# Kernel optimization log

Hardware: AMD Instinct MI355X
Metric: run time of the kernel (lower is better)

## Reference

```python
import jax, jax.numpy as jnp
import numpy as np

N_NODES = 100000
N_EDGES = 3200000
D = 256
REPEAT = 2
FACTOR = 0.5


def setup_inputs() -> dict:
    key = jax.random.key(0)
    k1, k2, k3, k4, k5, k6 = jax.random.split(key, 6)
    x = jax.random.normal(k1, (N_NODES, D), dtype=jnp.float32)
    vals = jax.random.uniform(k2, (N_EDGES,), dtype=jnp.float32)
    # Xavier-ish scale for linear weights
    W0 = jax.random.normal(k3, (D, D), dtype=jnp.float32) / np.sqrt(D)
    W1 = jax.random.normal(k4, (D, D), dtype=jnp.float32) / np.sqrt(D)
    rows = jax.random.randint(k5, (N_EDGES,), 0, N_NODES, dtype=jnp.int32)
    cols = jax.random.randint(k6, (N_EDGES,), 0, N_NODES, dtype=jnp.int32)
    return {"x": x, "vals": vals, "W0": W0, "W1": W1, "rows": rows, "cols": cols}


def reference(x, vals, W0, W1, rows, cols):
    # support is sparse [N, N] in COO: support[rows[e], cols[e]] = vals[e]
    def spmm(h):
        # gather source-node features, scale by edge weight, scatter-add to dst
        return jax.ops.segment_sum(vals[:, None] * h[cols], rows,
                                   num_segments=N_NODES)

    h = x
    for W, act in ((W0, jax.nn.relu), (W1, lambda v: v)):
        # _propagate: repeated SpMM with scalar factor
        for _ in range(REPEAT):
            h = spmm(h) * FACTOR
        # linear (no bias) + activation
        h = act(h @ W)
    return h
```

## Files before the change

kernel.cpp:

```cpp
#include <hip/hip_runtime.h>
#include <hip/hip_bf16.h>
#include <hip/hip_fp16.h>

#define N_D 256
#define NBLK 832
#define CPB 52
#define NCH 16
#define RPG_MAX 12512
#define EPB 4096
#define PR 512

typedef __attribute__((ext_vector_type(8))) short bf16x8;
typedef __attribute__((ext_vector_type(4))) float f32x4;

__device__ __forceinline__ unsigned short f2bf(float f) {
  union { float f; unsigned u; } c; c.f = f;
  unsigned u = c.u;
  return (unsigned short)((u + 0x7fffu + ((u >> 16) & 1u)) >> 16);
}
__device__ __forceinline__ float asf(unsigned u) {
  union { unsigned u; float f; } c; c.u = u;
  return c.f;
}
__device__ __forceinline__ int grp_of(int r, unsigned gmagic) {
  int g = (int)(((unsigned long long)(unsigned)r * gmagic) >> 37);
  return min(g, 7);
}
__device__ __forceinline__ unsigned packcv(int c, float vl) {
  const unsigned short hb = __half_as_ushort(__float2half_rn(vl * 0.5f));
  return ((unsigned)c << 15) | ((unsigned)hb >> 1);
}

template <bool AF32>
__device__ __forceinline__ void gemm_core(
    const void* __restrict__ H, const unsigned short* __restrict__ WT,
    unsigned short* __restrict__ C, int M, int bid) {
  const int wave = threadIdx.x >> 6;
  const int lane = threadIdx.x & 63;
  const int m = lane & 15;
  const int p = lane >> 4;
  const int row0 = bid * 128 + wave * 32;

  f32x4 acc0[16], acc1[16];
#pragma unroll
  for (int i = 0; i < 16; ++i) {
    acc0[i] = (f32x4){0.f, 0.f, 0.f, 0.f};
    acc1[i] = (f32x4){0.f, 0.f, 0.f, 0.f};
  }

  const int r0 = row0 + m;
  const int r1 = row0 + 16 + m;
  const bool ok0 = r0 < M, ok1 = r1 < M;

  for (int k0 = 0; k0 < N_D; k0 += 32) {
    bf16x8 a0 = {0,0,0,0,0,0,0,0}, a1 = {0,0,0,0,0,0,0,0};
    if (AF32) {
      if (ok0) {
        const float* ap = (const float*)H + (size_t)r0 * N_D + k0 + p * 8;
        const float4 f0 = *reinterpret_cast<const float4*>(ap);
        const float4 f1 = *reinterpret_cast<const float4*>(ap + 4);
        a0[0]=f2bf(f0.x); a0[1]=f2bf(f0.y); a0[2]=f2bf(f0.z); a0[3]=f2bf(f0.w);
        a0[4]=f2bf(f1.x); a0[5]=f2bf(f1.y); a0[6]=f2bf(f1.z); a0[7]=f2bf(f1.w);
      }
      if (ok1) {
        const float* ap = (const float*)H + (size_t)r1 * N_D + k0 + p * 8;
        const float4 f0 = *reinterpret_cast<const float4*>(ap);
        const float4 f1 = *reinterpret_cast<const float4*>(ap + 4);
        a1[0]=f2bf(f0.x); a1[1]=f2bf(f0.y); a1[2]=f2bf(f0.z); a1[3]=f2bf(f0.w);
        a1[4]=f2bf(f1.x); a1[5]=f2bf(f1.y); a1[6]=f2bf(f1.z); a1[7]=f2bf(f1.w);
      }
    } else {
      if (ok0) a0 = *reinterpret_cast<const bf16x8*>(
          (const unsigned short*)H + (size_t)r0 * N_D + k0 + p * 8);
      if (ok1) a1 = *reinterpret_cast<const bf16x8*>(
          (const unsigned short*)H + (size_t)r1 * N_D + k0 + p * 8);
    }
#pragma unroll
    for (int nt = 0; nt < 16; ++nt) {
      const bf16x8 b = *reinterpret_cast<const bf16x8*>(
          WT + (size_t)(nt * 16 + m) * N_D + k0 + p * 8);
      acc0[nt] = __builtin_amdgcn_mfma_f32_16x16x32_bf16(a0, b, acc0[nt], 0, 0, 0);
      acc1[nt] = __builtin_amdgcn_mfma_f32_16x16x32_bf16(a1, b, acc1[nt], 0, 0, 0);
    }
  }

#pragma unroll
  for (int nt = 0; nt < 16; ++nt) {
    const int col = nt * 16 + m;
#pragma unroll
    for (int rr = 0; rr < 4; ++rr) {
      const int ra = row0 + p * 4 + rr;
      const int rb = ra + 16;
      if (ra < M) C[(size_t)ra * N_D + col] = f2bf(acc0[nt][rr]);
      if (rb < M) C[(size_t)rb * N_D + col] = f2bf(acc1[nt][rr]);
    }
  }
}

__global__ __launch_bounds__(256) void gemm3_f32(
    const float* __restrict__ H, const unsigned short* __restrict__ WT,
    unsigned short* __restrict__ C, int M) {
  gemm_core<true>(H, WT, C, M, blockIdx.x);
}
__global__ __launch_bounds__(256) void gemm3_bf16(
    const unsigned short* __restrict__ H, const unsigned short* __restrict__ WT,
    unsigned short* __restrict__ C, int M) {
  gemm_core<false>(H, WT, C, M, blockIdx.x);
}

__global__ __launch_bounds__(256) void p0_kernel(
    const int* __restrict__ rows, int* __restrict__ cntT,
    int n_edges, unsigned gmagic,
    const float* __restrict__ W0, const float* __restrict__ W1,
    unsigned short* __restrict__ WT0, unsigned short* __restrict__ WT1) {
  if (blockIdx.x >= NBLK) {
    const int b = blockIdx.x - NBLK;
    const int w = b >> 8;
    const int k = b & 255;
    const int n = threadIdx.x;
    const float* W = w ? W1 : W0;
    unsigned short* WT = w ? WT1 : WT0;
    WT[(size_t)n * N_D + k] = f2bf(W[(size_t)k * N_D + n]);
    return;
  }
  __shared__ int l8[8];
  if (threadIdx.x < 8) l8[threadIdx.x] = 0;
  __syncthreads();
  const int e0 = blockIdx.x * EPB;
  const int e1 = min(n_edges, e0 + EPB);
  for (int e = e0 + threadIdx.x * 4; e < e1; e += 1024) {
    if (e + 3 < e1) {
      const int4 v = *reinterpret_cast<const int4*>(rows + e);
      atomicAdd(&l8[grp_of(v.x, gmagic)], 1);
      atomicAdd(&l8[grp_of(v.y, gmagic)], 1);
      atomicAdd(&l8[grp_of(v.z, gmagic)], 1);
      atomicAdd(&l8[grp_of(v.w, gmagic)], 1);
    } else {
      for (int k = 0; k < 4 && e + k < e1; ++k)
        atomicAdd(&l8[grp_of(rows[e + k], gmagic)], 1);
    }
  }
  __syncthreads();
  if (threadIdx.x < 8) cntT[threadIdx.x * NBLK + blockIdx.x] = l8[threadIdx.x];
}

__global__ __launch_bounds__(256) void scan_one(
    const int* __restrict__ in, int* __restrict__ out, int n) {
  __shared__ int swsum[4];
  __shared__ int carry_sh;
  const int tid = threadIdx.x;
  const int lane = tid & 63;
  const int wid = tid >> 6;
  if (tid == 0) carry_sh = 0;
  __syncthreads();
  for (int base = 0; base < n; base += 1024) {
    const int i0 = base + tid * 4;
    int4 v = make_int4(0, 0, 0, 0);
    if (i0 + 3 < n) v = *reinterpret_cast<const int4*>(in + i0);
    else {
      if (i0     < n) v.x = in[i0];
      if (i0 + 1 < n) v.y = in[i0 + 1];
      if (i0 + 2 < n) v.z = in[i0 + 2];
    }
    const int s1 = v.x, s2 = s1 + v.y, s3 = s2 + v.z, s4 = s3 + v.w;
    int ws = s4;
#pragma unroll
    for (int off = 1; off < 64; off <<= 1) {
      int o = __shfl_up(ws, off, 64);
      if (lane >= off) ws += o;
    }
    if (lane == 63) swsum[wid] = ws;
    __syncthreads();
    if (wid == 0) {
      int t = (lane < 4) ? swsum[lane] : 0;
#pragma unroll
      for (int off = 1; off < 4; off <<= 1) {
        int o = __shfl_up(t, off, 64);
        if (lane >= off) t += o;
      }
      if (lane < 4) swsum[lane] = t;
    }
    __syncthreads();
    const int carry = carry_sh;
    const int tbase = carry + (wid ? swsum[wid - 1] : 0) + ws - s4;
    if (i0     < n) out[i0]     = tbase;
    if (i0 + 1 < n) out[i0 + 1] = tbase + s1;
    if (i0 + 2 < n) out[i0 + 2] = tbase + s2;
    if (i0 + 3 < n) out[i0 + 3] = tbase + s3;
    __syncthreads();
    if (tid == 0) carry_sh = carry + swsum[3];
    __syncthreads();
  }
  if (tid == 0) out[n] = carry_sh;
}

__global__ __launch_bounds__(256) void partition_kernel(
    const int* __restrict__ rows, const int* __restrict__ cols,
    const float* __restrict__ vals, const int* __restrict__ pofsT,
    int2* __restrict__ part, int n_edges, unsigned gmagic) {
  __shared__ int lofs[8];
  __shared__ int lcnt[8];
  __shared__ int2 lbuf[8][PR];
  const int tid = threadIdx.x;
  const int bid = blockIdx.x;
  if (tid < 8) lofs[tid] = pofsT[tid * NBLK + bid];
  const int e0 = bid * EPB;
  const int e1 = min(n_edges, e0 + EPB);
  for (int base = e0; base < e1; base += PR) {
    if (tid < 8) lcnt[tid] = 0;
    __syncthreads();
    const int e = base + tid * 2;
    if (e < e1) {
      int2 rr, cc; float2 vv;
      const bool two = (e + 1 < e1);
      if (two) {
        rr = *reinterpret_cast<const int2*>(rows + e);
        cc = *reinterpret_cast<const int2*>(cols + e);
        vv = *reinterpret_cast<const float2*>(vals + e);
      } else {
        rr.x = rows[e]; cc.x = cols[e]; vv.x = vals[e];
      }
      {
        const int g = grp_of(rr.x, gmagic);
        const int slot = atomicAdd(&lcnt[g], 1);
        lbuf[g][slot] = make_int2(rr.x, (int)packcv(cc.x, vv.x));
      }
      if (two) {
        const int g = grp_of(rr.y, gmagic);
        const int slot = atomicAdd(&lcnt[g], 1);
        lbuf[g][slot] = make_int2(rr.y, (int)packcv(cc.y, vv.y));
      }
    }
    __syncthreads();
    for (int g = 0; g < 8; ++g) {
      const int c = lcnt[g];
      const int o = lofs[g];
      for (int i = tid; i < c; i += 256) part[o + i] = lbuf[g][i];
    }
    __syncthreads();
    if (tid < 8) lofs[tid] += lcnt[tid];
  }
}

__global__ __launch_bounds__(256) void hist_kernel(
    const int2* __restrict__ part, const int* __restrict__ pofsT,
    int* __restrict__ cntc, int M, int rpg) {
  const int g = blockIdx.x & 7;
  const int b = blockIdx.x >> 3;
  const int r0 = g * rpg;
  const int nr = min(rpg, M - r0);
  __shared__ int lh[RPG_MAX];
  for (int r = threadIdx.x; r < nr; r += 256) lh[r] = 0;
  __syncthreads();
  const int s0 = pofsT[g * NBLK + b * CPB];
  const int s1 = pofsT[g * NBLK + (b + 1) * CPB];
  for (int i = s0 + threadIdx.x; i < s1; i += 256) {
    atomicAdd(&lh[part[i].x - r0], 1);
  }
  __syncthreads();
  int* dst = cntc + (size_t)(g * NCH + b) * rpg;
  for (int r = threadIdx.x; r < nr; r += 256) dst[r] = lh[r];
}

__global__ __launch_bounds__(256) void sumcnt2_kernel(
    int* __restrict__ cntc, int* __restrict__ cnts,
    int* __restrict__ bsum, int M, int rpg) {
  __shared__ int wred[4];
  const int i = blockIdx.x * 256 + threadIdx.x;
  int s = 0;
  if (i < M) {
    const int g = i / rpg;
    const int rr = i - g * rpg;
    int* base = cntc + (size_t)g * NCH * rpg + rr;
#pragma unroll
    for (int b = 0; b < NCH; ++b) {
      const int c = base[(size_t)b * rpg];
      base[(size_t)b * rpg] = s;
      s += c;
    }
    cnts[i] = s;
  }
  int t = s;
#pragma unroll
  for (int off = 32; off; off >>= 1) t += __shfl_down(t, off, 64);
  if ((threadIdx.x & 63) == 0) wred[threadIdx.x >> 6] = t;
  __syncthreads();
  if (threadIdx.x == 0) bsum[blockIdx.x] = wred[0] + wred[1] + wred[2] + wred[3];
}

__global__ __launch_bounds__(256) void apply_kernel(
    const int* __restrict__ cnts, const int* __restrict__ bofs,
    int* __restrict__ row_ptr, int M) {
  __shared__ int wsum[4];
  const int tid = threadIdx.x;
  const int lane = tid & 63;
  const int wid = tid >> 6;
  const int i = blockIdx.x * 256 + tid;
  const int v = (i < M) ? cnts[i] : 0;
  int s = v;
#pragma unroll
  for (int off = 1; off < 64; off <<= 1) {
    int o = __shfl_up(s, off, 64);
    if (lane >= off) s += o;
  }
  if (lane == 63) wsum[wid] = s;
  __syncthreads();
  int add = 0;
  for (int k = 0; k < wid; ++k) add += wsum[k];
  const int excl = bofs[blockIdx.x] + add + s - v;
  if (i < M) row_ptr[i] = excl;
  if (i == M) row_ptr[M] = bofs[gridDim.x];
}

__global__ __launch_bounds__(256) void scatter3_kernel(
    const int2* __restrict__ part, const int* __restrict__ pofsT,
    const int* __restrict__ row_ptr, const int* __restrict__ cntc,
    unsigned* __restrict__ colpack, int M, int rpg) {
  const int g = blockIdx.x & 7;
  const int b = blockIdx.x >> 3;
  const int r0 = g * rpg;
  const int nr = min(rpg, M - r0);
  __shared__ int lc[RPG_MAX];
  const int* pfx = cntc + (size_t)(g * NCH + b) * rpg;
  for (int r = threadIdx.x; r < nr; r += 256)
    lc[r] = row_ptr[r0 + r] + pfx[r];
  __syncthreads();
  const int s0 = pofsT[g * NBLK + b * CPB];
  const int s1 = pofsT[g * NBLK + (b + 1) * CPB];
  for (int i = s0 + threadIdx.x; i < s1; i += 256) {
    const int2 rv = part[i];
    const int pos = atomicAdd(&lc[rv.x - r0], 1);
    colpack[pos] = (unsigned)rv.y;
  }
}

template <bool RELU, bool F32OUT>
__global__ __launch_bounds__(256) void spmm_slice(
    const unsigned short* __restrict__ hin, const int* __restrict__ row_ptr,
    const unsigned* __restrict__ colpack, void* __restrict__ hout,
    int n_nodes) {
  const int slice = blockIdx.x & 3;
  const int lane = threadIdx.x & 63;
  const int half = lane >> 5;
  const int sub  = lane & 31;
  const int wgid = ((blockIdx.x >> 2) * 256 + threadIdx.x) >> 6;
  const int node = wgid * 2 + half;
  const bool ok = node < n_nodes;
  int start = 0, end = 0;
  if (ok) { start = row_ptr[node]; end = row_ptr[node + 1]; }

  const unsigned* __restrict__ hinw = reinterpret_cast<const unsigned*>(hin);
  const int fofs = slice * 32 + sub;
  const int sbase = half << 5;

  float acc0 = 0.f, acc1 = 0.f;

  for (int base = start; base < end; base += 32) {
    const int cnt = min(32, end - base);
    unsigned u = 0;
    if (base + sub < end) u = __builtin_nontemporal_load(&colpack[base + sub]);
    for (int t = 0; t < cnt; t += 8) {
      unsigned hv[8];
      float v[8];
#pragma unroll
      for (int j = 0; j < 8; ++j) {
        const unsigned ue = (unsigned)__shfl((int)u, sbase + t + j, 64);
        const int c = (int)(ue >> 15);
        v[j] = __half2float(__ushort_as_half((unsigned short)(ue << 1)));
        hv[j] = hinw[(size_t)c * 128 + fofs];
      }
#pragma unroll
      for (int j = 0; j < 8; ++j) {
        acc0 += v[j] * asf(hv[j] << 16);
        acc1 += v[j] * asf(hv[j] & 0xffff0000u);
      }
    }
  }
  if (ok) {
    if (RELU) { acc0 = fmaxf(acc0, 0.f); acc1 = fmaxf(acc1, 0.f); }
    if (F32OUT) {
      reinterpret_cast<float2*>(hout)[(size_t)node * 128 + fofs] =
          make_float2(acc0, acc1);
    } else {
      reinterpret_cast<unsigned*>(hout)[(size_t)node * 128 + fofs] =
          (unsigned)f2bf(acc0) | ((unsigned)f2bf(acc1) << 16);
    }
  }
}

extern "C" void kernel_launch(void* const* d_in, const int* in_sizes, int n_in,
                              void* d_out, int out_size, void* d_ws, size_t ws_size,
                              hipStream_t stream) {
  const float* x    = (const float*)d_in[0];
  const float* vals = (const float*)d_in[1];
  const float* W0   = (const float*)d_in[2];
  const float* W1   = (const float*)d_in[3];
  const int*   rows = (const int*)d_in[4];
  const int*   cols = (const int*)d_in[5];

  const int n_edges = in_sizes[1];
  const int M = in_sizes[0] / N_D;
  const size_t n_feat = (size_t)M * N_D;

  char* ws = (char*)d_ws;
  unsigned short* hA      = (unsigned short*)(ws);
  unsigned*       colpack = (unsigned*)(ws + 51200000);
  int*            row_ptr = (int*)(ws + 64000000);
  int*            cnts    = (int*)(ws + 64400128);
  int*            bsum    = (int*)(ws + 64800256);
  int*            bofs    = (int*)(ws + 64802816);
  int*            cntT    = (int*)(ws + 64805376);
  int*            pofsT   = (int*)(ws + 64832000);
  unsigned short* wt0     = (unsigned short*)(ws + 64858880);
  unsigned short* wt1     = (unsigned short*)(ws + 64989952);
  unsigned short* hB   = (unsigned short*)d_out;
  unsigned short* hC   = (unsigned short*)d_out + n_feat;
  int2*           part = (int2*)((char*)d_out + 51200000);
  int*            cntc = (int*)((char*)d_out + 76800000);

  const int Mb = (M + 255) / 256;
  const int sblocks = 4 * ((M + 7) / 8);
  const int gblocks = (M + 127) / 128;
  const int rpg = (M + 7) / 8;
  const unsigned gmagic = (unsigned)(((1ULL << 37) + rpg - 1) / (unsigned long long)rpg);

  p0_kernel<<<NBLK + 512, 256, 0, stream>>>(rows, cntT, n_edges, gmagic,
                                            W0, W1, wt0, wt1);
  scan_one<<<1, 256, 0, stream>>>(cntT, pofsT, 8 * NBLK);
  gemm3_f32<<<gblocks, 256, 0, stream>>>(x, wt0, hB, M);
  partition_kernel<<<NBLK, 256, 0, stream>>>(rows, cols, vals, pofsT, part,
                                             n_edges, gmagic);
  hist_kernel<<<8 * NCH, 256, 0, stream>>>(part, pofsT, cntc, M, rpg);
  sumcnt2_kernel<<<Mb, 256, 0, stream>>>(cntc, cnts, bsum, M, rpg);
  scan_one<<<1, 256, 0, stream>>>(bsum, bofs, Mb);
  apply_kernel<<<Mb, 256, 0, stream>>>(cnts, bofs, row_ptr, M);
  scatter3_kernel<<<8 * NCH, 256, 0, stream>>>(part, pofsT, row_ptr, cntc,
                                               colpack, M, rpg);

  spmm_slice<false, false><<<sblocks, 256, 0, stream>>>(hB, row_ptr, colpack, hA, M);
  spmm_slice<true,  false><<<sblocks, 256, 0, stream>>>(hA, row_ptr, colpack, hB, M);

  gemm3_bf16<<<gblocks, 256, 0, stream>>>(hB, wt1, hC, M);
  spmm_slice<false, false><<<sblocks, 256, 0, stream>>>(hC, row_ptr, colpack, hA, M);
  spmm_slice<false, true ><<<sblocks, 256, 0, stream>>>(hA, row_ptr, colpack, d_out, M);
}
```

Before: 1.059 ms.

## Replace three-kernel row_ptr scan with per-group scan using partition offsets

Replaces the sumcnt/scan_one/apply kernel chain with a single 8-block groupscan kernel. Each block computes the degrees for its row group, scans them locally starting from the group's partition base offset in pofsT, and writes both row_ptr and absolute per-chunk offsets into cntc, so scatter no longer needs to read row_ptr. The GEMM A-operand loads also switch to nontemporal loads. This removes two launches and one grid-wide dependency, but the scan now runs on only 8 blocks with a serial per-thread chunk.

```diff
diff --git a/kernel.cpp b/kernel.cpp
--- a/kernel.cpp
+++ b/kernel.cpp
@@ -56,24 +56,24 @@
     bf16x8 a0 = {0,0,0,0,0,0,0,0}, a1 = {0,0,0,0,0,0,0,0};
     if (AF32) {
       if (ok0) {
-        const float* ap = (const float*)H + (size_t)r0 * N_D + k0 + p * 8;
-        const float4 f0 = *reinterpret_cast<const float4*>(ap);
-        const float4 f1 = *reinterpret_cast<const float4*>(ap + 4);
+        const f32x4* ap = (const f32x4*)((const float*)H + (size_t)r0 * N_D + k0 + p * 8);
+        const f32x4 f0 = __builtin_nontemporal_load(ap);
+        const f32x4 f1 = __builtin_nontemporal_load(ap + 1);
         a0[0]=f2bf(f0.x); a0[1]=f2bf(f0.y); a0[2]=f2bf(f0.z); a0[3]=f2bf(f0.w);
         a0[4]=f2bf(f1.x); a0[5]=f2bf(f1.y); a0[6]=f2bf(f1.z); a0[7]=f2bf(f1.w);
       }
       if (ok1) {
-        const float* ap = (const float*)H + (size_t)r1 * N_D + k0 + p * 8;
-        const float4 f0 = *reinterpret_cast<const float4*>(ap);
-        const float4 f1 = *reinterpret_cast<const float4*>(ap + 4);
+        const f32x4* ap = (const f32x4*)((const float*)H + (size_t)r1 * N_D + k0 + p * 8);
+        const f32x4 f0 = __builtin_nontemporal_load(ap);
+        const f32x4 f1 = __builtin_nontemporal_load(ap + 1);
         a1[0]=f2bf(f0.x); a1[1]=f2bf(f0.y); a1[2]=f2bf(f0.z); a1[3]=f2bf(f0.w);
         a1[4]=f2bf(f1.x); a1[5]=f2bf(f1.y); a1[6]=f2bf(f1.z); a1[7]=f2bf(f1.w);
       }
     } else {
-      if (ok0) a0 = *reinterpret_cast<const bf16x8*>(
-          (const unsigned short*)H + (size_t)r0 * N_D + k0 + p * 8);
-      if (ok1) a1 = *reinterpret_cast<const bf16x8*>(
-          (const unsigned short*)H + (size_t)r1 * N_D + k0 + p * 8);
+      if (ok0) a0 = __builtin_nontemporal_load(reinterpret_cast<const bf16x8*>(
+          (const unsigned short*)H + (size_t)r0 * N_D + k0 + p * 8));
+      if (ok1) a1 = __builtin_nontemporal_load(reinterpret_cast<const bf16x8*>(
+          (const unsigned short*)H + (size_t)r1 * N_D + k0 + p * 8));
     }
 #pragma unroll
     for (int nt = 0; nt < 16; ++nt) {
@@ -262,68 +262,76 @@
   for (int r = threadIdx.x; r < nr; r += 256) dst[r] = lh[r];
 }
 
-__global__ __launch_bounds__(256) void sumcnt2_kernel(
-    int* __restrict__ cntc, int* __restrict__ cnts,
-    int* __restrict__ bsum, int M, int rpg) {
-  __shared__ int wred[4];
-  const int i = blockIdx.x * 256 + threadIdx.x;
+__global__ __launch_bounds__(256) void groupscan_kernel(
+    int* __restrict__ cntc, const int* __restrict__ pofsT,
+    int* __restrict__ row_ptr, int M, int rpg) {
+  const int g = blockIdx.x;
+  const int r0 = g * rpg;
+  const int nr = min(rpg, M - r0);
+  __shared__ int deg[RPG_MAX];
+  __shared__ int tsum[256];
+  __shared__ int wq[4];
+  const int tid = threadIdx.x;
+  int* base = cntc + (size_t)g * NCH * rpg;
+  for (int r = tid; r < nr; r += 256) {
+    int s = 0;
+#pragma unroll
+    for (int b = 0; b < NCH; ++b) s += base[(size_t)b * rpg + r];
+    deg[r] = s;
+  }
+  __syncthreads();
+  const int CH = (nr + 255) / 256;
+  const int a0 = min(nr, tid * CH);
+  const int a1 = min(nr, a0 + CH);
   int s = 0;
-  if (i < M) {
-    const int g = i / rpg;
-    const int rr = i - g * rpg;
-    int* base = cntc + (size_t)g * NCH * rpg + rr;
+  for (int r = a0; r < a1; ++r) s += deg[r];
+  {
+    const int lane = tid & 63, wid = tid >> 6;
+    int sc = s;
+#pragma unroll
+    for (int off = 1; off < 64; off <<= 1) {
+      int o = __shfl_up(sc, off, 64);
+      if (lane >= off) sc += o;
+    }
+    if (lane == 63) wq[wid] = sc;
+    __syncthreads();
+    int add = 0;
+    for (int k = 0; k < wid; ++k) add += wq[k];
+    tsum[tid] = add + sc - s;
+  }
+  __syncthreads();
+  const int gbase = pofsT[g * NBLK];
+  int run = gbase + tsum[tid];
+  for (int r = a0; r < a1; ++r) {
+    const int d = deg[r];
+    deg[r] = run;
+    run += d;
+  }
+  __syncthreads();
+  for (int r = tid; r < nr; r += 256) {
+    int acc = deg[r];
+    row_ptr[r0 + r] = acc;
 #pragma unroll
     for (int b = 0; b < NCH; ++b) {
-      const int c = base[(size_t)b * rpg];
-      base[(size_t)b * rpg] = s;
-      s += c;
-    }
-    cnts[i] = s;
-  }
-  int t = s;
-#pragma unroll
-  for (int off = 32; off; off >>= 1) t += __shfl_down(t, off, 64);
-  if ((threadIdx.x & 63) == 0) wred[threadIdx.x >> 6] = t;
-  __syncthreads();
-  if (threadIdx.x == 0) bsum[blockIdx.x] = wred[0] + wred[1] + wred[2] + wred[3];
-}
-
-__global__ __launch_bounds__(256) void apply_kernel(
-    const int* __restrict__ cnts, const int* __restrict__ bofs,
-    int* __restrict__ row_ptr, int M) {
-  __shared__ int wsum[4];
-  const int tid = threadIdx.x;
-  const int lane = tid & 63;
-  const int wid = tid >> 6;
-  const int i = blockIdx.x * 256 + tid;
-  const int v = (i < M) ? cnts[i] : 0;
-  int s = v;
-#pragma unroll
-  for (int off = 1; off < 64; off <<= 1) {
-    int o = __shfl_up(s, off, 64);
-    if (lane >= off) s += o;
-  }
-  if (lane == 63) wsum[wid] = s;
-  __syncthreads();
-  int add = 0;
-  for (int k = 0; k < wid; ++k) add += wsum[k];
-  const int excl = bofs[blockIdx.x] + add + s - v;
-  if (i < M) row_ptr[i] = excl;
-  if (i == M) row_ptr[M] = bofs[gridDim.x];
+      const int c = base[(size_t)b * rpg + r];
+      base[(size_t)b * rpg + r] = acc;
+      acc += c;
+    }
+  }
+  if (g == 7 && tid == 0) row_ptr[M] = pofsT[8 * NBLK];
 }
 
 __global__ __launch_bounds__(256) void scatter3_kernel(
     const int2* __restrict__ part, const int* __restrict__ pofsT,
-    const int* __restrict__ row_ptr, const int* __restrict__ cntc,
-    unsigned* __restrict__ colpack, int M, int rpg) {
+    const int* __restrict__ cntc, unsigned* __restrict__ colpack,
+    int M, int rpg) {
   const int g = blockIdx.x & 7;
   const int b = blockIdx.x >> 3;
   const int r0 = g * rpg;
   const int nr = min(rpg, M - r0);
   __shared__ int lc[RPG_MAX];
   const int* pfx = cntc + (size_t)(g * NCH + b) * rpg;
-  for (int r = threadIdx.x; r < nr; r += 256)
-    lc[r] = row_ptr[r0 + r] + pfx[r];
+  for (int r = threadIdx.x; r < nr; r += 256) lc[r] = pfx[r];
   __syncthreads();
   const int s0 = pofsT[g * NBLK + b * CPB];
   const int s1 = pofsT[g * NBLK + (b + 1) * CPB];
@@ -406,9 +414,6 @@
   unsigned short* hA      = (unsigned short*)(ws);
   unsigned*       colpack = (unsigned*)(ws + 51200000);
   int*            row_ptr = (int*)(ws + 64000000);
-  int*            cnts    = (int*)(ws + 64400128);
-  int*            bsum    = (int*)(ws + 64800256);
-  int*            bofs    = (int*)(ws + 64802816);
   int*            cntT    = (int*)(ws + 64805376);
   int*            pofsT   = (int*)(ws + 64832000);
   unsigned short* wt0     = (unsigned short*)(ws + 64858880);
@@ -418,7 +423,6 @@
   int2*           part = (int2*)((char*)d_out + 51200000);
   int*            cntc = (int*)((char*)d_out + 76800000);
 
-  const int Mb = (M + 255) / 256;
   const int sblocks = 4 * ((M + 7) / 8);
   const int gblocks = (M + 127) / 128;
   const int rpg = (M + 7) / 8;
@@ -431,10 +435,8 @@
   partition_kernel<<<NBLK, 256, 0, stream>>>(rows, cols, vals, pofsT, part,
                                              n_edges, gmagic);
   hist_kernel<<<8 * NCH, 256, 0, stream>>>(part, pofsT, cntc, M, rpg);
-  sumcnt2_kernel<<<Mb, 256, 0, stream>>>(cntc, cnts, bsum, M, rpg);
-  scan_one<<<1, 256, 0, stream>>>(bsum, bofs, Mb);
-  apply_kernel<<<Mb, 256, 0, stream>>>(cnts, bofs, row_ptr, M);
-  scatter3_kernel<<<8 * NCH, 256, 0, stream>>>(part, pofsT, row_ptr, cntc,
+  groupscan_kernel<<<8, 256, 0, stream>>>(cntc, pofsT, row_ptr, M, rpg);
+  scatter3_kernel<<<8 * NCH, 256, 0, stream>>>(part, pofsT, cntc,
                                                colpack, M, rpg);
 
   spmm_slice<false, false><<<sblocks, 256, 0, stream>>>(hB, row_ptr, colpack, hA, M);
```

Result: slower. 1.115 ms (+5.3%).
